# Optimization experiments

Measured on AMD Instinct MI355X. Metric: run time of the kernel, lower is better.

The kernel has to match this reference:

```python
import jax, jax.numpy as jnp
import numpy as np
import math

D_MODEL = 1024
NHEAD = 16
HEAD_DIM = D_MODEL // NHEAD  # 64
FREQ = 10000.0


def _rope(x, freq=FREQ):
    # x: [B, H, S, D] with D even. Matches RotaryEmbedding.apply:
    # thetas = exp(-2*log(freq)*(i//2)/D) for i in [0, D/2)
    S, D = x.shape[-2], x.shape[-1]
    pos = jnp.arange(S, dtype=x.dtype)                       # [S]
    idx = jnp.arange(D // 2) // 2                            # floor(i/2)
    thetas = jnp.exp((-2.0 * math.log(freq) / D) * idx.astype(x.dtype))  # [D/2]
    ang = pos[:, None] * thetas[None, :]                     # [S, D/2]
    cos, sin = jnp.cos(ang), jnp.sin(ang)
    x2 = x.reshape(*x.shape[:-1], D // 2, 2)
    x0, x1 = x2[..., 0], x2[..., 1]
    out = jnp.stack([x0 * cos - x1 * sin, x0 * sin + x1 * cos], axis=-1)
    return out.reshape(x.shape)


def setup_inputs() -> dict:
    key = jax.random.key(0)
    k1, k2, k3, k4, k5 = jax.random.split(key, 5)
    B, S = 2, 2048
    scale = 1.0 / math.sqrt(D_MODEL)
    return {
        "embeddings": jax.random.normal(k1, (B, S, D_MODEL), dtype=jnp.float32),
        "W_qkv": jax.random.normal(k2, (D_MODEL, 3 * D_MODEL), dtype=jnp.float32) * scale,
        "b_qkv": jnp.zeros((3 * D_MODEL,), dtype=jnp.float32),
        "W_o": jax.random.normal(k4, (D_MODEL, D_MODEL), dtype=jnp.float32) * scale,
        "b_o": jnp.zeros((D_MODEL,), dtype=jnp.float32),
    }


def reference(embeddings, W_qkv, b_qkv, W_o, b_o):
    B, S, _ = embeddings.shape
    qkv = embeddings @ W_qkv + b_qkv                          # [B,S,3*D]
    q, k, v = jnp.split(qkv, 3, axis=-1)

    def split_heads(t):  # [B,S,D] -> [B,H,S,hd]
        return t.reshape(B, S, NHEAD, HEAD_DIM).transpose(0, 2, 1, 3)

    q, k, v = split_heads(q), split_heads(k), split_heads(v)
    q = _rope(q)
    k = _rope(k)

    scores = jnp.einsum("bhqd,bhkd->bhqk", q, k) / math.sqrt(HEAD_DIM)
    attn = jax.nn.softmax(scores, axis=-1)
    heads = jnp.einsum("bhqk,bhkd->bhqd", attn, v)            # [B,H,S,hd]
    out = heads.transpose(0, 2, 1, 3).reshape(B, S, D_MODEL)
    return out @ W_o + b_o
```

## Files before the change

### kernel.cpp

```cpp
#include <hip/hip_runtime.h>
#include <hip/hip_bf16.h>
#include <math.h>

typedef __bf16 bf16;
typedef __bf16 bf16x4 __attribute__((ext_vector_type(4)));
typedef __bf16 bf16x8 __attribute__((ext_vector_type(8)));
typedef float f32x4 __attribute__((ext_vector_type(4)));

#define DEV static __device__ __forceinline__

#define SS 2048
#define HH 16
#define HD 64

DEV void load_lds16(const bf16* g, bf16* l) {
  __builtin_amdgcn_global_load_lds(
      (const __attribute__((address_space(1))) unsigned int*)g,
      (__attribute__((address_space(3))) unsigned int*)l, 16, 0, 0);
}

#define MFMA(a, b, c) __builtin_amdgcn_mfma_f32_16x16x32_bf16(a, b, c, 0, 0, 0)

__global__ __launch_bounds__(256) void k_prep(
    const float* __restrict__ emb, bf16* __restrict__ Xb,
    const float* __restrict__ Wqkv, bf16* __restrict__ Wqt,
    const float* __restrict__ Wo, bf16* __restrict__ Wot) {
  __shared__ float tt[32][33];
  int bid = blockIdx.x;
  if (bid < 4096) {
    int i = (bid * 256 + threadIdx.x) * 4;
    float4 v = *reinterpret_cast<const float4*>(emb + i);
    bf16x4 o = {(bf16)v.x, (bf16)v.y, (bf16)v.z, (bf16)v.w};
    *reinterpret_cast<bf16x4*>(Xb + i) = o;
    return;
  }
  const float* in;
  bf16* out;
  int R = 1024, C, ctile, rtile;
  if (bid < 7168) {
    in = Wqkv; out = Wqt; C = 3072;
    int idx = bid - 4096; ctile = idx % 96; rtile = idx / 96;
  } else {
    in = Wo; out = Wot; C = 1024;
    int idx = bid - 7168; ctile = idx & 31; rtile = idx >> 5;
  }
  int tx = threadIdx.x & 31, ty = threadIdx.x >> 5;
#pragma unroll
  for (int i = 0; i < 4; ++i)
    tt[ty + 8 * i][tx] = in[(rtile * 32 + ty + 8 * i) * C + ctile * 32 + tx];
  __syncthreads();
#pragma unroll
  for (int i = 0; i < 4; ++i) {
    int oc = ctile * 32 + ty + 8 * i;
    out[oc * R + rtile * 32 + tx] = (bf16)tt[tx][ty + 8 * i];
  }
}

__global__ __launch_bounds__(512) void k_gemm1(
    const bf16* __restrict__ A, const bf16* __restrict__ Bt,
    const float* __restrict__ bias, bf16* __restrict__ Qo,
    bf16* __restrict__ Ko, bf16* __restrict__ Vt) {
  __shared__ bf16 As[2][16384];
  __shared__ bf16 Bs[2][16384];
  int wg = blockIdx.x;
  int xcd = wg & 7, idx = wg >> 3;
  int bm = (xcd & 3) * 4 + (idx & 3);
  int bn = (xcd >> 2) * 6 + (idx >> 2);
  int t = threadIdx.x, w = t >> 6, l = t & 63;
  int wm = w >> 2, wn = w & 3;
  int fr = l & 15, fg = l >> 4;
  const bf16* Ab = A + bm * 256 * 1024;
  const bf16* Bb = Bt + bn * 256 * 1024;
  int trow = t >> 3;
  const bf16* sA = Ab + trow * 1024 + (((t & 7) ^ (trow & 7)) * 8);
  const bf16* sB = Bb + trow * 1024 + (((t & 7) ^ (trow & 7)) * 8);
  int dst0 = (w << 9);
  int xo = fr & 7;

#define G1_STAGE(buf, ko)                                         \
  do {                                                            \
    _Pragma("unroll")                                             \
    for (int j = 0; j < 4; ++j) {                                 \
      load_lds16(sA + j * 65536 + (ko), &As[buf][j * 4096 + dst0]); \
      load_lds16(sB + j * 65536 + (ko), &Bs[buf][j * 4096 + dst0]); \
    }                                                             \
  } while (0)

  f32x4 acc[8][4];
#pragma unroll
  for (int mi = 0; mi < 8; ++mi)
#pragma unroll
    for (int ni = 0; ni < 4; ++ni) acc[mi][ni] = (f32x4){0.f, 0.f, 0.f, 0.f};

  G1_STAGE(0, 0);
  asm volatile("s_waitcnt vmcnt(0)" ::: "memory");
  __builtin_amdgcn_s_barrier();

  for (int kt = 0; kt < 16; ++kt) {
    int p = kt & 1;
    const bf16* Asb = &As[p][0];
    const bf16* Bsb = &Bs[p][0];
    if (kt < 15) G1_STAGE(p ^ 1, (kt + 1) * 64);
    bf16x8 av[8], bv[4];
#pragma unroll
    for (int ni = 0; ni < 4; ++ni)
      bv[ni] = *(const bf16x8*)(Bsb + (wn * 64 + ni * 16 + fr) * 64 + (fg ^ xo) * 8);
#pragma unroll
    for (int mi = 0; mi < 8; ++mi)
      av[mi] = *(const bf16x8*)(Asb + (wm * 128 + mi * 16 + fr) * 64 + (fg ^ xo) * 8);
    asm volatile("s_waitcnt lgkmcnt(0)" ::: "memory");
    __builtin_amdgcn_sched_barrier(0);
    __builtin_amdgcn_s_setprio(1);
#pragma unroll
    for (int mi = 0; mi < 8; ++mi)
#pragma unroll
      for (int ni = 0; ni < 4; ++ni)
        acc[mi][ni] = MFMA(av[mi], bv[ni], acc[mi][ni]);
    __builtin_amdgcn_s_setprio(0);
#pragma unroll
    for (int ni = 0; ni < 4; ++ni)
      bv[ni] = *(const bf16x8*)(Bsb + (wn * 64 + ni * 16 + fr) * 64 + ((4 + fg) ^ xo) * 8);
#pragma unroll
    for (int mi = 0; mi < 8; ++mi)
      av[mi] = *(const bf16x8*)(Asb + (wm * 128 + mi * 16 + fr) * 64 + ((4 + fg) ^ xo) * 8);
    asm volatile("s_waitcnt lgkmcnt(0)" ::: "memory");
    __builtin_amdgcn_sched_barrier(0);
    __builtin_amdgcn_s_setprio(1);
#pragma unroll
    for (int mi = 0; mi < 8; ++mi)
#pragma unroll
      for (int ni = 0; ni < 4; ++ni)
        acc[mi][ni] = MFMA(av[mi], bv[ni], acc[mi][ni]);
    __builtin_amdgcn_s_setprio(0);
    asm volatile("s_waitcnt vmcnt(0)" ::: "memory");
    __builtin_amdgcn_sched_barrier(0);
    __builtin_amdgcn_s_barrier();
  }
#pragma unroll
  for (int mi = 0; mi < 8; ++mi)
#pragma unroll
    for (int ni = 0; ni < 4; ++ni) {
      int gc = bn * 256 + wn * 64 + ni * 16 + fr;
      int sec = gc >> 10, cc = gc & 1023;
      int h = cc >> 6, d = cc & 63;
      float bb = bias[gc];
      int gr0 = bm * 256 + wm * 128 + mi * 16 + fg * 4;
      if (sec == 2) {
        int b0 = gr0 >> 11, s0 = gr0 & 2047;
        bf16x4 ov;
#pragma unroll
        for (int r = 0; r < 4; ++r) ov[r] = (bf16)(acc[mi][ni][r] + bb);
        *(bf16x4*)(Vt + (((long long)(b0 * HH + h)) * HD + d) * SS + s0) = ov;
      } else {
        bf16* dst = sec == 0 ? Qo : Ko;
#pragma unroll
        for (int r = 0; r < 4; ++r) {
          int gr = gr0 + r;
          int b = gr >> 11, s = gr & 2047;
          dst[((b * HH + h) * SS + s) * HD + d] = (bf16)(acc[mi][ni][r] + bb);
        }
      }
    }
#undef G1_STAGE
}

__global__ __launch_bounds__(256) void k_gemm2(
    const bf16* __restrict__ A, const bf16* __restrict__ Bt,
    const float* __restrict__ bias, float* __restrict__ out) {
  __shared__ bf16 As[2][8192];
  __shared__ bf16 Bs[2][8192];
  int wg = blockIdx.x;
  int xcd = wg & 7, idx = wg >> 3;
  int bm = xcd * 4 + (idx & 3);
  int bn = idx >> 2;
  int t = threadIdx.x, w = t >> 6, l = t & 63;
  int wm = w >> 1, wn = w & 1;
  int fr = l & 15, fg = l >> 4;
  const bf16* Ab = A + bm * 128 * 1024;
  const bf16* Bb = Bt + bn * 128 * 1024;
  int trow = t >> 3;
  const bf16* sA = Ab + trow * 1024 + (((t & 7) ^ (trow & 7)) * 8);
  const bf16* sB = Bb + trow * 1024 + (((t & 7) ^ (trow & 7)) * 8);
  int dst0 = (w << 9);
  int xo = fr & 7;

#define G2_STAGE(buf, ko)                                           \
  do {                                                              \
    _Pragma("unroll")                                               \
    for (int j = 0; j < 4; ++j) {                                   \
      load_lds16(sA + j * 32768 + (ko), &As[buf][j * 2048 + dst0]); \
      load_lds16(sB + j * 32768 + (ko), &Bs[buf][j * 2048 + dst0]); \
    }                                                               \
  } while (0)

  f32x4 acc[4][4];
#pragma unroll
  for (int mi = 0; mi < 4; ++mi)
#pragma unroll
    for (int ni = 0; ni < 4; ++ni) acc[mi][ni] = (f32x4){0.f, 0.f, 0.f, 0.f};

  G2_STAGE(0, 0);
  asm volatile("s_waitcnt vmcnt(0)" ::: "memory");
  __builtin_amdgcn_s_barrier();

  for (int kt = 0; kt < 16; ++kt) {
    int p = kt & 1;
    const bf16* Asb = &As[p][0];
    const bf16* Bsb = &Bs[p][0];
    if (kt < 15) G2_STAGE(p ^ 1, (kt + 1) * 64);
    bf16x8 av[4], bv[4];
#pragma unroll
    for (int ni = 0; ni < 4; ++ni)
      bv[ni] = *(const bf16x8*)(Bsb + (wn * 64 + ni * 16 + fr) * 64 + (fg ^ xo) * 8);
#pragma unroll
    for (int mi = 0; mi < 4; ++mi)
      av[mi] = *(const bf16x8*)(Asb + (wm * 64 + mi * 16 + fr) * 64 + (fg ^ xo) * 8);
    asm volatile("s_waitcnt lgkmcnt(0)" ::: "memory");
    __builtin_amdgcn_sched_barrier(0);
    __builtin_amdgcn_s_setprio(1);
#pragma unroll
    for (int mi = 0; mi < 4; ++mi)
#pragma unroll
      for (int ni = 0; ni < 4; ++ni)
        acc[mi][ni] = MFMA(av[mi], bv[ni], acc[mi][ni]);
    __builtin_amdgcn_s_setprio(0);
#pragma unroll
    for (int ni = 0; ni < 4; ++ni)
      bv[ni] = *(const bf16x8*)(Bsb + (wn * 64 + ni * 16 + fr) * 64 + ((4 + fg) ^ xo) * 8);
#pragma unroll
    for (int mi = 0; mi < 4; ++mi)
      av[mi] = *(const bf16x8*)(Asb + (wm * 64 + mi * 16 + fr) * 64 + ((4 + fg) ^ xo) * 8);
    asm volatile("s_waitcnt lgkmcnt(0)" ::: "memory");
    __builtin_amdgcn_sched_barrier(0);
    __builtin_amdgcn_s_setprio(1);
#pragma unroll
    for (int mi = 0; mi < 4; ++mi)
#pragma unroll
      for (int ni = 0; ni < 4; ++ni)
        acc[mi][ni] = MFMA(av[mi], bv[ni], acc[mi][ni]);
    __builtin_amdgcn_s_setprio(0);
    asm volatile("s_waitcnt vmcnt(0)" ::: "memory");
    __builtin_amdgcn_sched_barrier(0);
    __builtin_amdgcn_s_barrier();
  }
#pragma unroll
  for (int mi = 0; mi < 4; ++mi)
#pragma unroll
    for (int ni = 0; ni < 4; ++ni) {
      int gc = bn * 128 + wn * 64 + ni * 16 + fr;
      float bb = bias[gc];
      int gr0 = bm * 128 + wm * 64 + mi * 16 + fg * 4;
#pragma unroll
      for (int r = 0; r < 4; ++r)
        out[(gr0 + r) * 1024 + gc] = acc[mi][ni][r] + bb;
    }
#undef G2_STAGE
}

__global__ void k_rope(bf16* __restrict__ Qb, bf16* __restrict__ Kb) {
  int t = blockIdx.x * 256 + threadIdx.x;
  bf16* buf = (t >> 19) ? Kb : Qb;
  float qs = (t >> 19) ? 1.0f : 0.125f;
  int g = t & 524287;
  int j = g & 7;
  int s = (g >> 3) & 2047;
  bf16* p = buf + (long long)g * 8;
  const float CN = -0.28782313662425572f;
  float th0 = __expf(CN * (float)(2 * j));
  float th1 = __expf(CN * (float)(2 * j + 1));
  float sp = (float)s;
  float s0, c0, s1, c1;
  sincosf(sp * th0, &s0, &c0);
  sincosf(sp * th1, &s1, &c1);
  bf16x8 v = *(bf16x8*)p;
  float x[8];
#pragma unroll
  for (int i = 0; i < 8; ++i) x[i] = (float)v[i];
  float o[8];
  o[0] = x[0] * c0 - x[1] * s0; o[1] = x[0] * s0 + x[1] * c0;
  o[2] = x[2] * c0 - x[3] * s0; o[3] = x[2] * s0 + x[3] * c0;
  o[4] = x[4] * c1 - x[5] * s1; o[5] = x[4] * s1 + x[5] * c1;
  o[6] = x[6] * c1 - x[7] * s1; o[7] = x[6] * s1 + x[7] * c1;
  bf16x8 ov;
#pragma unroll
  for (int i = 0; i < 8; ++i) ov[i] = (bf16)(o[i] * qs);
  *(bf16x8*)p = ov;
}

__global__ __launch_bounds__(512) void k_attn(
    const bf16* __restrict__ Q, const bf16* __restrict__ K,
    const bf16* __restrict__ Vt, bf16* __restrict__ Hd) {
  __shared__ bf16 KVs[3][8192];
  __shared__ bf16 plds[8][16][72];
  int bid = blockIdx.x;
  int x = bid & 7, rr = bid >> 3;
  int bh = x * 4 + (rr & 3);
  int qt = rr >> 2;
  int b = bh >> 4, h = bh & 15;
  int t = threadIdx.x, w = t >> 6, l = t & 63;
  int fr = l & 15, fg = l >> 4;
  const bf16* Qb = Q + (long long)bh * SS * HD;
  const bf16* Kb = K + (long long)bh * SS * HD;
  const bf16* Vb = Vt + (long long)bh * HD * SS;
  bool isK = w < 4;
  int stride = isK ? 64 : 2048;
  int wrow = (isK ? w : (w - 4)) * 16 + (l >> 3);
  const bf16* src = (isK ? Kb : Vb) + wrow * stride + ((l & 7) ^ (l >> 3)) * 8;
  long long adv = isK ? 4096 : 64;
  int dbase = w * 1024;

  int q0 = qt * 128 + w * 16;
  bf16x8 qf0 = *(const bf16x8*)(Qb + (q0 + fr) * 64 + fg * 8);
  bf16x8 qf1 = *(const bf16x8*)(Qb + (q0 + fr) * 64 + 32 + fg * 8);
  f32x4 acc[4];
#pragma unroll
  for (int db = 0; db < 4; ++db) acc[db] = (f32x4){0.f, 0.f, 0.f, 0.f};
  float ssum = 0.f;
  const f32x4 zero = {0.f, 0.f, 0.f, 0.f};
  int xo = fr & 7;

#define ATTN_STAGE(BI, KV)                                          \
  do {                                                              \
    load_lds16(src + (long long)(KV) * adv, &KVs[BI][dbase]);       \
    load_lds16(src + (long long)(KV) * adv + 8 * stride,            \
               &KVs[BI][dbase + 512]);                              \
  } while (0)

#define ATTN_COMPUTE(Ksp, Vsp)                                               \
  do {                                                                       \
    f32x4 stl[4];                                                            \
    __builtin_amdgcn_s_setprio(1);                                           \
    _Pragma("unroll")                                                        \
    for (int ks = 0; ks < 4; ++ks) {                                         \
      bf16x8 k0 = *(const bf16x8*)((Ksp) + (ks * 16 + fr) * 64 + (fg ^ xo) * 8); \
      bf16x8 k1 = *(const bf16x8*)((Ksp) + (ks * 16 + fr) * 64 + ((4 + fg) ^ xo) * 8); \
      stl[ks] = MFMA(k0, qf0, zero);                                         \
      stl[ks] = MFMA(k1, qf1, stl[ks]);                                      \
    }                                                                        \
    __builtin_amdgcn_s_setprio(0);                                           \
    float ps = 0.f;                                                          \
    _Pragma("unroll")                                                        \
    for (int ks = 0; ks < 4; ++ks) {                                         \
      bf16x4 pb;                                                             \
      _Pragma("unroll")                                                      \
      for (int r = 0; r < 4; ++r) {                                          \
        float p = __expf(stl[ks][r] - 16.0f);                                \
        ps += p;                                                             \
        pb[r] = (bf16)p;                                                     \
      }                                                                      \
      *(bf16x4*)&plds[w][fr][ks * 16 + fg * 4] = pb;                         \
    }                                                                        \
    ssum += ps;                                                              \
    bf16x8 pf0 = *(const bf16x8*)&plds[w][fr][fg * 8];                       \
    bf16x8 pf1 = *(const bf16x8*)&plds[w][fr][32 + fg * 8];                  \
    __builtin_amdgcn_s_setprio(1);                                           \
    _Pragma("unroll")                                                        \
    for (int db = 0; db < 4; ++db) {                                         \
      bf16x8 vf0 = *(const bf16x8*)((Vsp) + (db * 16 + fr) * 64 + (fg ^ xo) * 8); \
      bf16x8 vf1 = *(const bf16x8*)((Vsp) + (db * 16 + fr) * 64 + ((4 + fg) ^ xo) * 8); \
      acc[db] = MFMA(vf0, pf0, acc[db]);                                     \
      acc[db] = MFMA(vf1, pf1, acc[db]);                                     \
    }                                                                        \
    __builtin_amdgcn_s_setprio(0);                                           \
  } while (0)

  ATTN_STAGE(0, 0);
  ATTN_STAGE(1, 1);

  int cb = 0;
  int sb = 2;
  for (int it = 0; it < 31; ++it) {
    asm volatile("s_waitcnt vmcnt(2)" ::: "memory");
    __builtin_amdgcn_s_barrier();
    __builtin_amdgcn_sched_barrier(0);
    if (it < 30) ATTN_STAGE(sb, it + 2);
    const bf16* Ks = &KVs[cb][0];
    const bf16* Vs = &KVs[cb][4096];
    ATTN_COMPUTE(Ks, Vs);
    cb = cb == 2 ? 0 : cb + 1;
    sb = sb == 2 ? 0 : sb + 1;
  }
  asm volatile("s_waitcnt vmcnt(0)" ::: "memory");
  __builtin_amdgcn_s_barrier();
  __builtin_amdgcn_sched_barrier(0);
  {
    const bf16* Ks = &KVs[cb][0];
    const bf16* Vs = &KVs[cb][4096];
    ATTN_COMPUTE(Ks, Vs);
  }
  float sv = ssum;
  sv += __shfl_xor(sv, 16);
  sv += __shfl_xor(sv, 32);
  float inv = 1.0f / sv;
  int s = q0 + fr;
#pragma unroll
  for (int db = 0; db < 4; ++db) {
    bf16x4 ob;
#pragma unroll
    for (int r = 0; r < 4; ++r) ob[r] = (bf16)(acc[db][r] * inv);
    *(bf16x4*)(Hd + ((long long)(b * SS + s)) * 1024 + h * 64 + db * 16 + fg * 4) = ob;
  }
#undef ATTN_STAGE
#undef ATTN_COMPUTE
}

extern "C" void kernel_launch(void* const* d_in, const int* in_sizes, int n_in,
                              void* d_out, int out_size, void* d_ws, size_t ws_size,
                              hipStream_t stream) {
  const float* emb = (const float*)d_in[0];
  const float* Wqkv = (const float*)d_in[1];
  const float* bqkv = (const float*)d_in[2];
  const float* Wo = (const float*)d_in[3];
  const float* bo = (const float*)d_in[4];
  float* out = (float*)d_out;
  char* ws = (char*)d_ws;
  bf16* Xb  = (bf16*)(ws);
  bf16* Wqt = (bf16*)(ws + 8388608);
  bf16* Wot = (bf16*)(ws + 14680064);
  bf16* Qb  = (bf16*)(ws + 16777216);
  bf16* Kb  = (bf16*)(ws + 25165824);
  bf16* Vt  = (bf16*)(ws + 41943040);
  bf16* Hd  = (bf16*)(ws + 50331648);

  hipLaunchKernelGGL(k_prep, dim3(8192), dim3(256), 0, stream, emb, Xb, Wqkv, Wqt, Wo, Wot);
  hipLaunchKernelGGL(k_gemm1, dim3(192), dim3(512), 0, stream, Xb, Wqt, bqkv, Qb, Kb, Vt);
  hipLaunchKernelGGL(k_rope, dim3(4096), dim3(256), 0, stream, Qb, Kb);
  hipLaunchKernelGGL(k_attn, dim3(512), dim3(512), 0, stream, Qb, Kb, Vt, Hd);
  hipLaunchKernelGGL(k_gemm2, dim3(256), dim3(256), 0, stream, Hd, Wot, bo, out);
}
```

Before: 129.4 us.

## Retile QKV GEMM to 256x192 for full CU coverage and fuse Q RoPE into attention

The QKV projection GEMM moves from 256x256 to 256x192 tiles, so the grid grows from 192 to 256 workgroups and matches the 256 CUs of the device. RoPE and the 1/8 scaling for Q now run inside the attention kernel on the Q fragments held in registers, so the standalone RoPE pass only handles K and Q no longer makes an extra global read/write round trip. In exchange, each GEMM tile reuses its A data over fewer columns, and every attention block recomputes sincos for its Q rows.

```diff
diff --git a/kernel.cpp b/kernel.cpp
--- a/kernel.cpp
+++ b/kernel.cpp
@@ -61,36 +61,37 @@
     const float* __restrict__ bias, bf16* __restrict__ Qo,
     bf16* __restrict__ Ko, bf16* __restrict__ Vt) {
   __shared__ bf16 As[2][16384];
-  __shared__ bf16 Bs[2][16384];
+  __shared__ bf16 Bs[2][12288];
   int wg = blockIdx.x;
   int xcd = wg & 7, idx = wg >> 3;
   int bm = (xcd & 3) * 4 + (idx & 3);
-  int bn = (xcd >> 2) * 6 + (idx >> 2);
+  int bn = (xcd >> 2) * 8 + (idx >> 2);
   int t = threadIdx.x, w = t >> 6, l = t & 63;
   int wm = w >> 2, wn = w & 3;
   int fr = l & 15, fg = l >> 4;
   const bf16* Ab = A + bm * 256 * 1024;
-  const bf16* Bb = Bt + bn * 256 * 1024;
+  const bf16* Bb = Bt + bn * 192 * 1024;
   int trow = t >> 3;
   const bf16* sA = Ab + trow * 1024 + (((t & 7) ^ (trow & 7)) * 8);
   const bf16* sB = Bb + trow * 1024 + (((t & 7) ^ (trow & 7)) * 8);
   int dst0 = (w << 9);
   int xo = fr & 7;
 
-#define G1_STAGE(buf, ko)                                         \
-  do {                                                            \
-    _Pragma("unroll")                                             \
-    for (int j = 0; j < 4; ++j) {                                 \
+#define G1_STAGE(buf, ko)                                           \
+  do {                                                              \
+    _Pragma("unroll")                                               \
+    for (int j = 0; j < 4; ++j)                                     \
       load_lds16(sA + j * 65536 + (ko), &As[buf][j * 4096 + dst0]); \
+    _Pragma("unroll")                                               \
+    for (int j = 0; j < 3; ++j)                                     \
       load_lds16(sB + j * 65536 + (ko), &Bs[buf][j * 4096 + dst0]); \
-    }                                                             \
   } while (0)
 
-  f32x4 acc[8][4];
+  f32x4 acc[8][3];
 #pragma unroll
   for (int mi = 0; mi < 8; ++mi)
 #pragma unroll
-    for (int ni = 0; ni < 4; ++ni) acc[mi][ni] = (f32x4){0.f, 0.f, 0.f, 0.f};
+    for (int ni = 0; ni < 3; ++ni) acc[mi][ni] = (f32x4){0.f, 0.f, 0.f, 0.f};
 
   G1_STAGE(0, 0);
   asm volatile("s_waitcnt vmcnt(0)" ::: "memory");
@@ -101,10 +102,10 @@
     const bf16* Asb = &As[p][0];
     const bf16* Bsb = &Bs[p][0];
     if (kt < 15) G1_STAGE(p ^ 1, (kt + 1) * 64);
-    bf16x8 av[8], bv[4];
-#pragma unroll
-    for (int ni = 0; ni < 4; ++ni)
-      bv[ni] = *(const bf16x8*)(Bsb + (wn * 64 + ni * 16 + fr) * 64 + (fg ^ xo) * 8);
+    bf16x8 av[8], bv[3];
+#pragma unroll
+    for (int ni = 0; ni < 3; ++ni)
+      bv[ni] = *(const bf16x8*)(Bsb + (wn * 48 + ni * 16 + fr) * 64 + (fg ^ xo) * 8);
 #pragma unroll
     for (int mi = 0; mi < 8; ++mi)
       av[mi] = *(const bf16x8*)(Asb + (wm * 128 + mi * 16 + fr) * 64 + (fg ^ xo) * 8);
@@ -114,12 +115,12 @@
 #pragma unroll
     for (int mi = 0; mi < 8; ++mi)
 #pragma unroll
-      for (int ni = 0; ni < 4; ++ni)
+      for (int ni = 0; ni < 3; ++ni)
         acc[mi][ni] = MFMA(av[mi], bv[ni], acc[mi][ni]);
     __builtin_amdgcn_s_setprio(0);
 #pragma unroll
-    for (int ni = 0; ni < 4; ++ni)
-      bv[ni] = *(const bf16x8*)(Bsb + (wn * 64 + ni * 16 + fr) * 64 + ((4 + fg) ^ xo) * 8);
+    for (int ni = 0; ni < 3; ++ni)
+      bv[ni] = *(const bf16x8*)(Bsb + (wn * 48 + ni * 16 + fr) * 64 + ((4 + fg) ^ xo) * 8);
 #pragma unroll
     for (int mi = 0; mi < 8; ++mi)
       av[mi] = *(const bf16x8*)(Asb + (wm * 128 + mi * 16 + fr) * 64 + ((4 + fg) ^ xo) * 8);
@@ -129,7 +130,7 @@
 #pragma unroll
     for (int mi = 0; mi < 8; ++mi)
 #pragma unroll
-      for (int ni = 0; ni < 4; ++ni)
+      for (int ni = 0; ni < 3; ++ni)
         acc[mi][ni] = MFMA(av[mi], bv[ni], acc[mi][ni]);
     __builtin_amdgcn_s_setprio(0);
     asm volatile("s_waitcnt vmcnt(0)" ::: "memory");
@@ -139,8 +140,8 @@
 #pragma unroll
   for (int mi = 0; mi < 8; ++mi)
 #pragma unroll
-    for (int ni = 0; ni < 4; ++ni) {
-      int gc = bn * 256 + wn * 64 + ni * 16 + fr;
+    for (int ni = 0; ni < 3; ++ni) {
+      int gc = bn * 192 + wn * 48 + ni * 16 + fr;
       int sec = gc >> 10, cc = gc & 1023;
       int h = cc >> 6, d = cc & 63;
       float bb = bias[gc];
@@ -257,14 +258,11 @@
 #undef G2_STAGE
 }
 
-__global__ void k_rope(bf16* __restrict__ Qb, bf16* __restrict__ Kb) {
+__global__ void k_rope(bf16* __restrict__ Kb) {
   int t = blockIdx.x * 256 + threadIdx.x;
-  bf16* buf = (t >> 19) ? Kb : Qb;
-  float qs = (t >> 19) ? 1.0f : 0.125f;
-  int g = t & 524287;
-  int j = g & 7;
-  int s = (g >> 3) & 2047;
-  bf16* p = buf + (long long)g * 8;
+  int j = t & 7;
+  int s = (t >> 3) & 2047;
+  bf16* p = Kb + (long long)t * 8;
   const float CN = -0.28782313662425572f;
   float th0 = __expf(CN * (float)(2 * j));
   float th1 = __expf(CN * (float)(2 * j + 1));
@@ -283,7 +281,7 @@
   o[6] = x[6] * c1 - x[7] * s1; o[7] = x[6] * s1 + x[7] * c1;
   bf16x8 ov;
 #pragma unroll
-  for (int i = 0; i < 8; ++i) ov[i] = (bf16)(o[i] * qs);
+  for (int i = 0; i < 8; ++i) ov[i] = (bf16)o[i];
   *(bf16x8*)p = ov;
 }
 
@@ -312,6 +310,32 @@
   int q0 = qt * 128 + w * 16;
   bf16x8 qf0 = *(const bf16x8*)(Qb + (q0 + fr) * 64 + fg * 8);
   bf16x8 qf1 = *(const bf16x8*)(Qb + (q0 + fr) * 64 + 32 + fg * 8);
+  {
+    const float CN = -0.28782313662425572f;
+    float sp = (float)(q0 + fr);
+    float s0, c0, s1, c1, s2, c2, s3, c3;
+    sincosf(sp * __expf(CN * (float)(2 * fg)), &s0, &c0);
+    sincosf(sp * __expf(CN * (float)(2 * fg + 1)), &s1, &c1);
+    sincosf(sp * __expf(CN * (float)(8 + 2 * fg)), &s2, &c2);
+    sincosf(sp * __expf(CN * (float)(9 + 2 * fg)), &s3, &c3);
+    float xq[8], oq[8];
+#pragma unroll
+    for (int i = 0; i < 8; ++i) xq[i] = (float)qf0[i];
+    oq[0] = xq[0] * c0 - xq[1] * s0; oq[1] = xq[0] * s0 + xq[1] * c0;
+    oq[2] = xq[2] * c0 - xq[3] * s0; oq[3] = xq[2] * s0 + xq[3] * c0;
+    oq[4] = xq[4] * c1 - xq[5] * s1; oq[5] = xq[4] * s1 + xq[5] * c1;
+    oq[6] = xq[6] * c1 - xq[7] * s1; oq[7] = xq[6] * s1 + xq[7] * c1;
+#pragma unroll
+    for (int i = 0; i < 8; ++i) qf0[i] = (bf16)(oq[i] * 0.125f);
+#pragma unroll
+    for (int i = 0; i < 8; ++i) xq[i] = (float)qf1[i];
+    oq[0] = xq[0] * c2 - xq[1] * s2; oq[1] = xq[0] * s2 + xq[1] * c2;
+    oq[2] = xq[2] * c2 - xq[3] * s2; oq[3] = xq[2] * s2 + xq[3] * c2;
+    oq[4] = xq[4] * c3 - xq[5] * s3; oq[5] = xq[4] * s3 + xq[5] * c3;
+    oq[6] = xq[6] * c3 - xq[7] * s3; oq[7] = xq[6] * s3 + xq[7] * c3;
+#pragma unroll
+    for (int i = 0; i < 8; ++i) qf1[i] = (bf16)(oq[i] * 0.125f);
+  }
   f32x4 acc[4];
 #pragma unroll
   for (int db = 0; db < 4; ++db) acc[db] = (f32x4){0.f, 0.f, 0.f, 0.f};
@@ -423,8 +447,8 @@
   bf16* Hd  = (bf16*)(ws + 50331648);
 
   hipLaunchKernelGGL(k_prep, dim3(8192), dim3(256), 0, stream, emb, Xb, Wqkv, Wqt, Wo, Wot);
-  hipLaunchKernelGGL(k_gemm1, dim3(192), dim3(512), 0, stream, Xb, Wqt, bqkv, Qb, Kb, Vt);
-  hipLaunchKernelGGL(k_rope, dim3(4096), dim3(256), 0, stream, Qb, Kb);
+  hipLaunchKernelGGL(k_gemm1, dim3(256), dim3(512), 0, stream, Xb, Wqt, bqkv, Qb, Kb, Vt);
+  hipLaunchKernelGGL(k_rope, dim3(2048), dim3(256), 0, stream, Kb);
   hipLaunchKernelGGL(k_attn, dim3(512), dim3(512), 0, stream, Qb, Kb, Vt, Hd);
   hipLaunchKernelGGL(k_gemm2, dim3(256), dim3(256), 0, stream, Hd, Wot, bo, out);
 }
```

Result: faster. 119.7 us (-7.5%).
